# Kernel optimization log

Measured on AMD Instinct MI355X. Metric: run time of the kernel, lower is better.

The kernel has to match this reference:

```python
import jax, jax.numpy as jnp
import numpy as np

B, LA, LQ, LO, H, OUT = 32, 2048, 64, 32, 1024, 5


def _kaiming(key, out_f, in_f):
    return jax.random.normal(key, (out_f, in_f), jnp.float32) * np.sqrt(2.0 / in_f)


def setup_inputs() -> dict:
    key = jax.random.key(0)
    ks = jax.random.split(key, 16)
    inp = {
        "article_contexts": jax.random.normal(ks[0], (B, LA, H), jnp.float32),
        "question_contexts": jax.random.normal(ks[1], (B, LQ, H), jnp.float32),
        "options_embeds": jax.random.normal(ks[2], (B, 5, LO, H), jnp.float32),
        "answer_indices": jax.random.randint(ks[3], (B,), 0, LQ),
    }
    # mlp_att (article-question attention) params
    inp["a_Qw"], inp["a_Qb"] = _kaiming(ks[4], H, H), jnp.zeros((H,), jnp.float32)
    inp["a_Kw"], inp["a_Kb"] = _kaiming(ks[5], H, H), jnp.zeros((H,), jnp.float32)
    inp["a_Vw"], inp["a_Vb"] = _kaiming(ks[6], H, H), jnp.zeros((H,), jnp.float32)
    inp["a_vw"], inp["a_vb"] = _kaiming(ks[7], 1, H), jnp.zeros((1,), jnp.float32)
    # dot_layer (option attention) params
    inp["d_Qw"], inp["d_Qb"] = _kaiming(ks[8], H, H), jnp.zeros((H,), jnp.float32)
    inp["d_Kw"], inp["d_Kb"] = _kaiming(ks[9], H, H), jnp.zeros((H,), jnp.float32)
    inp["d_Vw"], inp["d_Vb"] = _kaiming(ks[10], H, H), jnp.zeros((H,), jnp.float32)
    inp["d_vw"], inp["d_vb"] = _kaiming(ks[11], 1, H), jnp.zeros((1,), jnp.float32)
    # final linear: hidden_size*5 -> output_dim
    inp["f_w"], inp["f_b"] = _kaiming(ks[12], OUT, 5 * H), jnp.zeros((OUT,), jnp.float32)
    return inp


def _mlp_att(Q, K, V, Qw, Qb, Kw, Kb, Vw, Vb, vw, vb):
    # Q: [B, H]; K, V: [B, (..opt..), L, H]. Dropout is identity (eval mode).
    Qp = Q @ Qw.T + Qb                      # [B, H]
    Kp = K @ Kw.T + Kb                      # [..., L, H]
    Vp = V @ Vw.T + Vb                      # [..., L, H]
    while Qp.ndim < Kp.ndim:
        Qp = Qp[..., None, :]
    M = jnp.tanh(Qp + Kp)                   # [..., L, H]
    scores = jax.nn.softmax(M @ vw.T + vb, axis=-2)  # softmax over L, [..., L, 1]
    return jnp.sum(Vp * scores, axis=-2)    # [..., H]


def reference(article_contexts, question_contexts, options_embeds, answer_indices,
              a_Qw, a_Qb, a_Kw, a_Kb, a_Vw, a_Vb, a_vw, a_vb,
              d_Qw, d_Qb, d_Kw, d_Kb, d_Vw, d_Vb, d_vw, d_vb,
              f_w, f_b):
    b = article_contexts.shape[0]
    # gather question context at the answer index -> [B, H]
    oqc = question_contexts[jnp.arange(b), answer_indices]
    # article-question additive attention -> [B, H]
    aq = _mlp_att(oqc, article_contexts, article_contexts,
                  a_Qw, a_Qb, a_Kw, a_Kb, a_Vw, a_Vb, a_vw, a_vb)
    # per-option additive attention, vectorized over the 5 options -> [B, 5, H]
    feats = _mlp_att(aq, options_embeds, options_embeds,
                     d_Qw, d_Qb, d_Kw, d_Kb, d_Vw, d_Vb, d_vw, d_vb)
    # concat options along feature dim, final linear -> [B, OUT]
    logits = feats.reshape(b, -1) @ f_w.T + f_b
    return logits
```

## Files before the change

kernel.cpp:

```cpp
#include <hip/hip_runtime.h>
#include <hip/hip_bf16.h>
#include <math.h>

#define HDIM 1024
#define NB 32
#define LA 2048
#define LO 32

typedef __attribute__((ext_vector_type(8))) short bf16x8;
typedef __attribute__((ext_vector_type(4))) float f32x4;
typedef unsigned int u32;

__device__ __forceinline__ float tanh_fast(float x){
    return 2.0f / (1.0f + __expf(-2.0f * x)) - 1.0f;
}

__device__ __forceinline__ void load_lds16(const void* gptr, void* lptr){
    __builtin_amdgcn_global_load_lds(
        (const __attribute__((address_space(1))) u32*)gptr,
        (__attribute__((address_space(3))) u32*)lptr, 16, 0, 0);
}

__device__ __forceinline__ void conv_range(const float* __restrict__ in,
                                           __hip_bfloat16* __restrict__ out,
                                           long n, int nblk, int lb){
    long i = ((long)lb * 256 + threadIdx.x) * 4;
    long stride = (long)nblk * 256 * 4;
    for (; i < n; i += stride){
        float4 v = *(const float4*)(in + i);
        union { __hip_bfloat16 h[4]; short4 s; } u;
        u.h[0] = __float2bfloat16(v.x); u.h[1] = __float2bfloat16(v.y);
        u.h[2] = __float2bfloat16(v.z); u.h[3] = __float2bfloat16(v.w);
        *(short4*)(out + i) = u.s;
    }
}

__global__ __launch_bounds__(256) void mega_init_kernel(
    const float* __restrict__ article, __hip_bfloat16* __restrict__ art_bf,
    float* __restrict__ zbase,
    const float* __restrict__ question, const int* __restrict__ ans,
    const float* __restrict__ a_Qw, const float* __restrict__ a_Qb,
    float* __restrict__ qp_a,
    const float* __restrict__ a_Kw, __hip_bfloat16* __restrict__ kwa_bf,
    const float* __restrict__ d_Kw, __hip_bfloat16* __restrict__ kwd_bf,
    const float* __restrict__ options, __hip_bfloat16* __restrict__ opt_bf)
{
    __shared__ float xin[HDIM];
    int bid = blockIdx.x;
    const int tid = threadIdx.x;
    if (bid < 1024){ conv_range(article, art_bf, 67108864L, 1024, bid); return; }
    bid -= 1024;
    if (bid < 32){
        int i = bid * 256 + tid;
        for (; i < 103424; i += 8192) zbase[i] = 0.f;
        return;
    }
    bid -= 32;
    if (bid < 512){
        const int g = bid >> 4, yq = bid & 15;
        const int lane = tid & 63, wave = tid >> 6;
        const float* in = question + ((size_t)g * 64 + ans[g]) * HDIM;
        *(float4*)&xin[tid * 4] = *(const float4*)&in[tid * 4];
        __syncthreads();
        float4 xv[4];
        #pragma unroll
        for (int c = 0; c < 4; c++) xv[c] = *(const float4*)&xin[(c * 64 + lane) * 4];
        const int hbase = yq * 64 + wave * 16;
        #pragma unroll 4
        for (int r = 0; r < 16; r++){
            int h = hbase + r;
            const float* Wr = a_Qw + (size_t)h * HDIM;
            float p = 0.f;
            #pragma unroll
            for (int c = 0; c < 4; c++){
                float4 wv = *(const float4*)&Wr[(c * 64 + lane) * 4];
                p = fmaf(xv[c].x, wv.x, p); p = fmaf(xv[c].y, wv.y, p);
                p = fmaf(xv[c].z, wv.z, p); p = fmaf(xv[c].w, wv.w, p);
            }
            #pragma unroll
            for (int off = 1; off < 64; off <<= 1) p += __shfl_xor(p, off, 64);
            if (lane == 0) qp_a[(size_t)g * HDIM + h] = p + a_Qb[h];
        }
        return;
    }
    bid -= 512;
    if (bid < 64){ conv_range(a_Kw, kwa_bf, 1048576L, 64, bid); return; }
    bid -= 64;
    if (bid < 64){ conv_range(d_Kw, kwd_bf, 1048576L, 64, bid); return; }
    bid -= 64;
    conv_range(options, opt_bf, 5242880L, 320, bid);
}

__global__ __launch_bounds__(256) void proj_kernel(
    const float* __restrict__ in, const float* __restrict__ W,
    const float* __restrict__ bias, float* __restrict__ out){
    __shared__ float xin[HDIM];
    const int g = blockIdx.x, tid = threadIdx.x;
    const int lane = tid & 63, wave = tid >> 6;
    *(float4*)&xin[tid * 4] = *(const float4*)&in[(size_t)g * HDIM + tid * 4];
    __syncthreads();
    float4 xv[4];
    #pragma unroll
    for (int c = 0; c < 4; c++) xv[c] = *(const float4*)&xin[(c * 64 + lane) * 4];
    const int hbase = blockIdx.y * 64 + wave * 16;
    #pragma unroll 4
    for (int r = 0; r < 16; r++){
        int h = hbase + r;
        const float* Wr = W + (size_t)h * HDIM;
        float p = 0.f;
        #pragma unroll
        for (int c = 0; c < 4; c++){
            float4 wv = *(const float4*)&Wr[(c * 64 + lane) * 4];
            p = fmaf(xv[c].x, wv.x, p); p = fmaf(xv[c].y, wv.y, p);
            p = fmaf(xv[c].z, wv.z, p); p = fmaf(xv[c].w, wv.w, p);
        }
        #pragma unroll
        for (int off = 1; off < 64; off <<= 1) p += __shfl_xor(p, off, 64);
        if (lane == 0) out[(size_t)g * HDIM + h] = p + bias[h];
    }
}

__global__ __launch_bounds__(512, 2) void score_mfma8p(
    const __hip_bfloat16* __restrict__ X, const __hip_bfloat16* __restrict__ Kw,
    const float* __restrict__ Kb, const float* __restrict__ Qp,
    const float* __restrict__ vw, float* __restrict__ s,
    int rows_per_batch)
{
    __shared__ __align__(16) char lds[131072];
    const int tid = threadIdx.x;
    const int lane = tid & 63, wid = tid >> 6;
    const int wm = wid >> 2, wn = wid & 3;
    const int lr = lane & 15, lg = lane >> 4;

    const int na = gridDim.x >> 2;
    const int bid = blockIdx.x;
    const int xcd = bid & 7, seq = bid >> 3;
    const int a_idx = xcd * (na >> 3) + (seq >> 2);
    const int h_idx = seq & 3;
    const int a0 = a_idx * 256, h0 = h_idx * 256;

    f32x4 acc[8][4] = {};
    bf16x8 av[8], bv[4];

    const int rA = tid >> 2;
    const int csw = ((tid & 3) * 16) ^ (((rA >> 1) & 3) << 4);
    const char* pA = (const char*)Kw + (size_t)(h0 + rA) * 2048 + csw;
    const char* pB = (const char*)X  + (size_t)(a0 + rA) * 2048 + csw;
    char* dst0 = lds + tid * 16;

    int aoff[8], boff[4];
    #pragma unroll
    for (int hf = 0; hf < 8; hf++){
        int rw = wm * 128 + hf * 16 + lr;
        aoff[hf] = rw * 64 + ((lg * 16) ^ (((rw >> 1) & 3) << 4));
    }
    #pragma unroll
    for (int af = 0; af < 4; af++){
        int rw = wn * 64 + af * 16 + lr;
        boff[af] = 16384 + rw * 64 + ((lg * 16) ^ (((rw >> 1) & 3) << 4));
    }

#define ISSUE_PAIR(j) do { \
    const int _base = (((j) >> 1) & 1) * 65536 + ((j) & 1) * 32768; \
    const size_t _ko = (size_t)(((j) >> 1) * 128 + ((j) & 1) * 64); \
    load_lds16(pA + _ko, dst0 + _base); \
    load_lds16(pA + _ko + 262144, dst0 + _base + 8192); \
    load_lds16(pB + _ko, dst0 + _base + 16384); \
    load_lds16(pB + _ko + 262144, dst0 + _base + 24576); } while(0)

#define READS_PAIR(k) do { \
    const int _base = (((k) >> 1) & 1) * 65536 + ((k) & 1) * 32768; \
    _Pragma("unroll") \
    for (int hf = 0; hf < 8; hf++) av[hf] = *(const bf16x8*)(lds + _base + aoff[hf]); \
    _Pragma("unroll") \
    for (int af = 0; af < 4; af++) bv[af] = *(const bf16x8*)(lds + _base + boff[af]); } while(0)

#define MFMA32() do { \
    asm volatile("s_waitcnt lgkmcnt(0)" ::: "memory"); \
    __builtin_amdgcn_sched_barrier(0); \
    __builtin_amdgcn_s_setprio(1); \
    _Pragma("unroll") \
    for (int hf = 0; hf < 8; hf++) \
        _Pragma("unroll") \
        for (int af = 0; af < 4; af++) \
            acc[hf][af] = __builtin_amdgcn_mfma_f32_16x16x32_bf16(av[hf], bv[af], acc[hf][af], 0, 0, 0); \
    __builtin_amdgcn_s_setprio(0); } while(0)

    ISSUE_PAIR(0); ISSUE_PAIR(1); ISSUE_PAIR(2);

    #pragma unroll 2
    for (int k = 0; k < 29; ++k){
        asm volatile("s_waitcnt vmcnt(8)" ::: "memory");
        __builtin_amdgcn_s_barrier();
        ISSUE_PAIR(k + 3);
        READS_PAIR(k);
        MFMA32();
    }
    {
        asm volatile("s_waitcnt vmcnt(8)" ::: "memory");
        __builtin_amdgcn_s_barrier();
        READS_PAIR(29);
        MFMA32();
    }
    {
        asm volatile("s_waitcnt vmcnt(4)" ::: "memory");
        __builtin_amdgcn_s_barrier();
        READS_PAIR(30);
        MFMA32();
    }
    {
        asm volatile("s_waitcnt vmcnt(0)" ::: "memory");
        __builtin_amdgcn_s_barrier();
        READS_PAIR(31);
        MFMA32();
    }

    const int b = a0 / rows_per_batch;
    float part[4] = {0.f, 0.f, 0.f, 0.f};
    #pragma unroll
    for (int hf = 0; hf < 8; hf++){
        int hbase = h0 + wm * 128 + hf * 16 + lg * 4;
        float4 kb4 = *(const float4*)(Kb + hbase);
        float4 qp4 = *(const float4*)(Qp + (size_t)b * HDIM + hbase);
        float4 vw4 = *(const float4*)(vw + hbase);
        float q0v = kb4.x + qp4.x, q1v = kb4.y + qp4.y;
        float q2v = kb4.z + qp4.z, q3v = kb4.w + qp4.w;
        #pragma unroll
        for (int af = 0; af < 4; af++){
            part[af] += tanh_fast(acc[hf][af][0] + q0v) * vw4.x;
            part[af] += tanh_fast(acc[hf][af][1] + q1v) * vw4.y;
            part[af] += tanh_fast(acc[hf][af][2] + q2v) * vw4.z;
            part[af] += tanh_fast(acc[hf][af][3] + q3v) * vw4.w;
        }
    }
    #pragma unroll
    for (int af = 0; af < 4; af++){
        float p = part[af];
        p += __shfl_xor(p, 16, 64);
        p += __shfl_xor(p, 32, 64);
        if (lane < 16)
            atomicAdd(&s[a0 + wn * 64 + af * 16 + lr], p);
    }
#undef ISSUE_PAIR
#undef READS_PAIR
#undef MFMA32
}

#define SBM 128
#define SBN 128
__global__ __launch_bounds__(256) void score_mfma_kernel(
    const __hip_bfloat16* __restrict__ X, const __hip_bfloat16* __restrict__ Kw,
    const float* __restrict__ Kb, const float* __restrict__ Qp,
    const float* __restrict__ vw, float* __restrict__ s,
    int row_off, int rows_per_batch)
{
    __shared__ __align__(16) __hip_bfloat16 As[SBM][32];
    __shared__ __align__(16) __hip_bfloat16 Bs[SBN][32];
    const int tid = threadIdx.x;
    const int lane = tid & 63, wid = tid >> 6;
    const int wm = wid >> 1, wn = wid & 1;
    const int row0 = blockIdx.x * SBM;
    const int h0 = blockIdx.y * SBN;
    const int lr = lane & 15, lg = lane >> 4;

    f32x4 acc[4][4] = {};

    for (int k0 = 0; k0 < HDIM; k0 += 32){
        #pragma unroll
        for (int l = 0; l < 2; l++){
            int f = tid + l * 256;
            int r = f >> 2, c8 = (f & 3) * 8;
            load_lds16(X + (size_t)(row0 + r) * HDIM + k0 + c8, &As[0][0] + f * 8);
            load_lds16(Kw + (size_t)(h0 + r) * HDIM + k0 + c8, &Bs[0][0] + f * 8);
        }
        __syncthreads();
        bf16x8 a[4], b[4];
        #pragma unroll
        for (int i = 0; i < 4; i++)
            a[i] = *(const bf16x8*)&As[wm * 64 + i * 16 + lr][lg * 8];
        #pragma unroll
        for (int j = 0; j < 4; j++)
            b[j] = *(const bf16x8*)&Bs[wn * 64 + j * 16 + lr][lg * 8];
        #pragma unroll
        for (int i = 0; i < 4; i++)
            #pragma unroll
            for (int j = 0; j < 4; j++)
                acc[i][j] = __builtin_amdgcn_mfma_f32_16x16x32_bf16(a[i], b[j], acc[i][j], 0, 0, 0);
        __syncthreads();
    }

    float kbv[4], vwv[4];
    #pragma unroll
    for (int j = 0; j < 4; j++){
        int h = h0 + wn * 64 + j * 16 + lr;
        kbv[j] = Kb[h]; vwv[j] = vw[h];
    }
    #pragma unroll
    for (int i = 0; i < 4; i++){
        #pragma unroll
        for (int reg = 0; reg < 4; reg++){
            int r = row0 + wm * 64 + i * 16 + lg * 4 + reg;
            int gr = row_off + r;
            int bb = gr / rows_per_batch;
            const float* Qpb = Qp + (size_t)bb * HDIM;
            float p = 0.f;
            #pragma unroll
            for (int j = 0; j < 4; j++){
                int h = h0 + wn * 64 + j * 16 + lr;
                p += tanh_fast(acc[i][j][reg] + kbv[j] + Qpb[h]) * vwv[j];
            }
            #pragma unroll
            for (int off = 1; off < 16; off <<= 1) p += __shfl_xor(p, off, 16);
            if (lr == 0) atomicAdd(&s[gr], p);
        }
    }
}

__global__ void softmax_kernel(float* __restrict__ s, int Rg){
    __shared__ float red[4];
    int g = blockIdx.x, tid = threadIdx.x;
    float* sg = s + (size_t)g * Rg;
    float m = -INFINITY;
    for (int i = tid; i < Rg; i += 256) m = fmaxf(m, sg[i]);
    #pragma unroll
    for (int off = 32; off > 0; off >>= 1) m = fmaxf(m, __shfl_down(m, off, 64));
    if ((tid & 63) == 0) red[tid >> 6] = m;
    __syncthreads();
    m = fmaxf(fmaxf(red[0], red[1]), fmaxf(red[2], red[3]));
    __syncthreads();
    float sum = 0.f;
    for (int i = tid; i < Rg; i += 256){ float e = __expf(sg[i] - m); sg[i] = e; sum += e; }
    #pragma unroll
    for (int off = 32; off > 0; off >>= 1) sum += __shfl_down(sum, off, 64);
    if ((tid & 63) == 0) red[tid >> 6] = sum;
    __syncthreads();
    float inv = 1.0f / (red[0] + red[1] + red[2] + red[3]);
    for (int i = tid; i < Rg; i += 256) sg[i] *= inv;
}

__global__ __launch_bounds__(256) void wsum_art_v(
    const __hip_bfloat16* __restrict__ X, const float* __restrict__ sc,
    float* __restrict__ out){
    __shared__ float scs[256];
    const int g = blockIdx.x, ic = blockIdx.y, tid = threadIdx.x;
    scs[tid] = sc[(size_t)g * LA + ic * 256 + tid];
    __syncthreads();
    const __hip_bfloat16* Xg = X + ((size_t)g * LA + ic * 256) * HDIM + tid * 4;
    float a0 = 0.f, a1 = 0.f, a2 = 0.f, a3 = 0.f;
    for (int i = 0; i < 256; i++){
        short4 v = *(const short4*)(Xg + (size_t)i * HDIM);
        float w = scs[i];
        a0 = fmaf(w, __bfloat162float(*(const __hip_bfloat16*)&v.x), a0);
        a1 = fmaf(w, __bfloat162float(*(const __hip_bfloat16*)&v.y), a1);
        a2 = fmaf(w, __bfloat162float(*(const __hip_bfloat16*)&v.z), a2);
        a3 = fmaf(w, __bfloat162float(*(const __hip_bfloat16*)&v.w), a3);
    }
    float* o = out + (size_t)g * HDIM + tid * 4;
    atomicAdd(o + 0, a0); atomicAdd(o + 1, a1);
    atomicAdd(o + 2, a2); atomicAdd(o + 3, a3);
}

__global__ __launch_bounds__(256) void wsum_opt_sm(
    const __hip_bfloat16* __restrict__ X, const float* __restrict__ sraw,
    float* __restrict__ out){
    __shared__ float raw[LO], scs[LO];
    const int g = blockIdx.x, tid = threadIdx.x;
    if (tid < LO) raw[tid] = sraw[(size_t)g * LO + tid];
    __syncthreads();
    float m = -INFINITY;
    #pragma unroll
    for (int i = 0; i < LO; i++) m = fmaxf(m, raw[i]);
    float ssum = 0.f;
    #pragma unroll
    for (int i = 0; i < LO; i++) ssum += __expf(raw[i] - m);
    if (tid < LO) scs[tid] = __expf(raw[tid] - m) / ssum;
    __syncthreads();
    const __hip_bfloat16* Xg = X + (size_t)g * LO * HDIM + tid * 4;
    float a0 = 0.f, a1 = 0.f, a2 = 0.f, a3 = 0.f;
    for (int i = 0; i < LO; i++){
        short4 v = *(const short4*)(Xg + (size_t)i * HDIM);
        float w = scs[i];
        a0 = fmaf(w, __bfloat162float(*(const __hip_bfloat16*)&v.x), a0);
        a1 = fmaf(w, __bfloat162float(*(const __hip_bfloat16*)&v.y), a1);
        a2 = fmaf(w, __bfloat162float(*(const __hip_bfloat16*)&v.z), a2);
        a3 = fmaf(w, __bfloat162float(*(const __hip_bfloat16*)&v.w), a3);
    }
    float* o = out + (size_t)g * HDIM + tid * 4;
    o[0] = a0; o[1] = a1; o[2] = a2; o[3] = a3;
}

__global__ void final_kernel(const float* __restrict__ feats, const float* __restrict__ fw,
                             const float* __restrict__ fb, float* __restrict__ out){
    __shared__ float red[4];
    int b = blockIdx.x, tid = threadIdx.x;
    const float* fe = feats + (size_t)b * 5120;
    for (int j = 0; j < 5; j++){
        float acc = 0.f;
        for (int i = tid; i < 5120; i += 256) acc += fe[i] * fw[(size_t)j * 5120 + i];
        #pragma unroll
        for (int off = 32; off > 0; off >>= 1) acc += __shfl_down(acc, off, 64);
        if ((tid & 63) == 0) red[tid >> 6] = acc;
        __syncthreads();
        if (tid == 0) out[b * 5 + j] = fb[j] + red[0] + red[1] + red[2] + red[3];
        __syncthreads();
    }
}

extern "C" void kernel_launch(void* const* d_in, const int* in_sizes, int n_in,
                              void* d_out, int out_size, void* d_ws, size_t ws_size,
                              hipStream_t stream) {
    const float* article  = (const float*)d_in[0];
    const float* question = (const float*)d_in[1];
    const float* options  = (const float*)d_in[2];
    const int*   ans      = (const int*)d_in[3];
    const float* a_Qw = (const float*)d_in[4];  const float* a_Qb = (const float*)d_in[5];
    const float* a_Kw = (const float*)d_in[6];  const float* a_Kb = (const float*)d_in[7];
    const float* a_Vw = (const float*)d_in[8];  const float* a_Vb = (const float*)d_in[9];
    const float* a_vw = (const float*)d_in[10];
    const float* d_Qw = (const float*)d_in[12]; const float* d_Qb = (const float*)d_in[13];
    const float* d_Kw = (const float*)d_in[14]; const float* d_Kb = (const float*)d_in[15];
    const float* d_Vw = (const float*)d_in[16]; const float* d_Vb = (const float*)d_in[17];
    const float* d_vw = (const float*)d_in[18];
    const float* f_w  = (const float*)d_in[20]; const float* f_b  = (const float*)d_in[21];
    float* out = (float*)d_out;

    float* ws = (float*)d_ws;
    float* qp_a  = ws + 32768;
    float* aq    = ws + 65536;
    float* qp_d  = ws + 98304;
    float* feats = ws + 131072;
    float* s_art = ws + 294912;
    float* s_opt = ws + 360448;
    float* w_art = ws + 365568;
    float* wd    = ws + 398336;
    __hip_bfloat16* kwa_bf = (__hip_bfloat16*)(ws + 562176);
    __hip_bfloat16* kwd_bf = kwa_bf + 1048576;
    __hip_bfloat16* opt_bf = kwd_bf + 1048576;
    __hip_bfloat16* art_bf = opt_bf + 5242880;

    mega_init_kernel<<<2016, 256, 0, stream>>>(
        article, art_bf, s_art,
        question, ans, a_Qw, a_Qb, qp_a,
        a_Kw, kwa_bf, d_Kw, kwd_bf, options, opt_bf);
    score_mfma8p<<<(NB * LA / 256) * 4, 512, 0, stream>>>(
        art_bf, kwa_bf, a_Kb, qp_a, a_vw, s_art, LA);
    softmax_kernel<<<NB, 256, 0, stream>>>(s_art, LA);
    wsum_art_v<<<dim3(NB, 8), 256, 0, stream>>>(art_bf, s_art, w_art);
    proj_kernel<<<dim3(NB, 16), 256, 0, stream>>>(w_art, a_Vw, a_Vb, aq);
    proj_kernel<<<dim3(NB, 16), 256, 0, stream>>>(aq, d_Qw, d_Qb, qp_d);
    score_mfma_kernel<<<dim3((NB * 5 * LO) / SBM, HDIM / SBN), 256, 0, stream>>>(
        opt_bf, kwd_bf, d_Kb, qp_d, d_vw, s_opt, 0, 5 * LO);
    wsum_opt_sm<<<NB * 5, 256, 0, stream>>>(opt_bf, s_opt, wd);
    proj_kernel<<<dim3(NB * 5, 16), 256, 0, stream>>>(wd, d_Vw, d_Vb, feats);
    final_kernel<<<NB, 256, 0, stream>>>(feats, f_w, f_b, out);
}
```

Baseline: 399.7 us.

## Split main GEMM loop into two barrier-separated phases with staggered loads

Restructures the K-loop of the score GEMM into two half-phases per k-step, each doing LDS reads for half the A fragments, issuing half of the next global-to-LDS loads, then running half the MFMAs between barriers. This resembles a ping-pong style schedule meant to interleave memory issue with MFMA work across waves and spread vmcnt waits. It adds extra barriers per iteration and changes the vmcnt accounting, which risks more synchronization stalls or a hazard if the counts are wrong.

```diff
diff --git a/kernel.cpp b/kernel.cpp
--- a/kernel.cpp
+++ b/kernel.cpp
@@ -160,59 +160,76 @@
         boff[af] = 16384 + rw * 64 + ((lg * 16) ^ (((rw >> 1) & 3) << 4));
     }
 
+#define PBASE(j) ((((j) >> 1) & 1) * 65536 + ((j) & 1) * 32768)
+#define PKOFF(j) ((size_t)(((j) >> 1) * 128 + ((j) & 1) * 64))
 #define ISSUE_PAIR(j) do { \
-    const int _base = (((j) >> 1) & 1) * 65536 + ((j) & 1) * 32768; \
-    const size_t _ko = (size_t)(((j) >> 1) * 128 + ((j) & 1) * 64); \
-    load_lds16(pA + _ko, dst0 + _base); \
-    load_lds16(pA + _ko + 262144, dst0 + _base + 8192); \
-    load_lds16(pB + _ko, dst0 + _base + 16384); \
-    load_lds16(pB + _ko + 262144, dst0 + _base + 24576); } while(0)
-
-#define READS_PAIR(k) do { \
-    const int _base = (((k) >> 1) & 1) * 65536 + ((k) & 1) * 32768; \
-    _Pragma("unroll") \
-    for (int hf = 0; hf < 8; hf++) av[hf] = *(const bf16x8*)(lds + _base + aoff[hf]); \
-    _Pragma("unroll") \
-    for (int af = 0; af < 4; af++) bv[af] = *(const bf16x8*)(lds + _base + boff[af]); } while(0)
-
-#define MFMA32() do { \
+    load_lds16(pA + PKOFF(j), dst0 + PBASE(j)); \
+    load_lds16(pA + PKOFF(j) + 262144, dst0 + PBASE(j) + 8192); \
+    load_lds16(pB + PKOFF(j), dst0 + PBASE(j) + 16384); \
+    load_lds16(pB + PKOFF(j) + 262144, dst0 + PBASE(j) + 24576); } while(0)
+#define ISSUE_A(j) do { \
+    load_lds16(pA + PKOFF(j), dst0 + PBASE(j)); \
+    load_lds16(pA + PKOFF(j) + 262144, dst0 + PBASE(j) + 8192); } while(0)
+#define ISSUE_B(j) do { \
+    load_lds16(pB + PKOFF(j), dst0 + PBASE(j) + 16384); \
+    load_lds16(pB + PKOFF(j) + 262144, dst0 + PBASE(j) + 24576); } while(0)
+
+#define WAIT_LGKM() do { \
     asm volatile("s_waitcnt lgkmcnt(0)" ::: "memory"); \
-    __builtin_amdgcn_sched_barrier(0); \
+    __builtin_amdgcn_sched_barrier(0); } while(0)
+#define BAR() __builtin_amdgcn_s_barrier()
+
+#define MFMA_HALF(H0) do { \
     __builtin_amdgcn_s_setprio(1); \
     _Pragma("unroll") \
-    for (int hf = 0; hf < 8; hf++) \
+    for (int hf = (H0); hf < (H0) + 4; hf++) \
         _Pragma("unroll") \
         for (int af = 0; af < 4; af++) \
             acc[hf][af] = __builtin_amdgcn_mfma_f32_16x16x32_bf16(av[hf], bv[af], acc[hf][af], 0, 0, 0); \
     __builtin_amdgcn_s_setprio(0); } while(0)
 
+#define PHASE_A(k, DO_ISSUE) do { \
+    const int _b = PBASE(k); \
+    _Pragma("unroll") \
+    for (int hf = 0; hf < 4; hf++) av[hf] = *(const bf16x8*)(lds + _b + aoff[hf]); \
+    _Pragma("unroll") \
+    for (int af = 0; af < 4; af++) bv[af] = *(const bf16x8*)(lds + _b + boff[af]); \
+    if (DO_ISSUE) ISSUE_A((k) + 3); \
+    BAR(); \
+    WAIT_LGKM(); \
+    MFMA_HALF(0); \
+    BAR(); } while(0)
+
+#define PHASE_B(k, DO_ISSUE, VMC) do { \
+    const int _b = PBASE(k); \
+    _Pragma("unroll") \
+    for (int hf = 4; hf < 8; hf++) av[hf] = *(const bf16x8*)(lds + _b + aoff[hf]); \
+    if (DO_ISSUE) ISSUE_B((k) + 3); \
+    asm volatile("s_waitcnt vmcnt(" #VMC ")" ::: "memory"); \
+    BAR(); \
+    WAIT_LGKM(); \
+    MFMA_HALF(4); \
+    BAR(); } while(0)
+
     ISSUE_PAIR(0); ISSUE_PAIR(1); ISSUE_PAIR(2);
-
-    #pragma unroll 2
-    for (int k = 0; k < 29; ++k){
-        asm volatile("s_waitcnt vmcnt(8)" ::: "memory");
-        __builtin_amdgcn_s_barrier();
-        ISSUE_PAIR(k + 3);
-        READS_PAIR(k);
-        MFMA32();
-    }
+    asm volatile("s_waitcnt vmcnt(8)" ::: "memory");
+    BAR();
+
+    #pragma unroll 4
+    for (int k = 0; k < 28; ++k){
+        PHASE_A(k, 1);
+        PHASE_B(k, 1, 8);
+    }
+    PHASE_A(28, 1); PHASE_B(28, 1, 8);
+    PHASE_A(29, 0); PHASE_B(29, 0, 4);
+    PHASE_A(30, 0); PHASE_B(30, 0, 0);
+    PHASE_A(31, 0);
     {
-        asm volatile("s_waitcnt vmcnt(8)" ::: "memory");
-        __builtin_amdgcn_s_barrier();
-        READS_PAIR(29);
-        MFMA32();
-    }
-    {
-        asm volatile("s_waitcnt vmcnt(4)" ::: "memory");
-        __builtin_amdgcn_s_barrier();
-        READS_PAIR(30);
-        MFMA32();
-    }
-    {
-        asm volatile("s_waitcnt vmcnt(0)" ::: "memory");
-        __builtin_amdgcn_s_barrier();
-        READS_PAIR(31);
-        MFMA32();
+        const int _b = PBASE(31);
+        #pragma unroll
+        for (int hf = 4; hf < 8; hf++) av[hf] = *(const bf16x8*)(lds + _b + aoff[hf]);
+        WAIT_LGKM();
+        MFMA_HALF(4);
     }
 
     const int b = a0 / rows_per_batch;
@@ -241,9 +258,16 @@
         if (lane < 16)
             atomicAdd(&s[a0 + wn * 64 + af * 16 + lr], p);
     }
+#undef PBASE
+#undef PKOFF
 #undef ISSUE_PAIR
-#undef READS_PAIR
-#undef MFMA32
+#undef ISSUE_A
+#undef ISSUE_B
+#undef WAIT_LGKM
+#undef BAR
+#undef MFMA_HALF
+#undef PHASE_A
+#undef PHASE_B
 }
 
 #define SBM 128
```

Result: no change. 397.2 us (-0.6%).
